# Performance work log

Hardware: AMD Instinct MI355X
Metric: run time of the kernel (lower is better)

The kernel has to match this reference:

```python
import jax, jax.numpy as jnp
import numpy as np

D_MODEL = 1024
NUM_HEADS = 16
DK = D_MODEL // NUM_HEADS  # 64


def setup_inputs() -> dict:
    key = jax.random.key(0)
    kx, kq, kk, kv, ko = jax.random.split(key, 5)
    B, S = 4, 2048
    # xavier-uniform-ish scale for square [d_model, d_model] matrices
    bound = float(np.sqrt(6.0 / (D_MODEL + D_MODEL)))
    uni = lambda k: jax.random.uniform(k, (D_MODEL, D_MODEL), jnp.float32, -bound, bound)
    return {
        "x": jax.random.normal(kx, (B, S, D_MODEL), jnp.float32),
        "q_heads": uni(kq),
        "k_heads": uni(kk),
        "v_heads": uni(kv),
        "output_proj": uni(ko),
    }


def reference(x, q_heads, k_heads, v_heads, output_proj):
    B, S, _ = x.shape
    # projections: x @ W.T, split into heads -> [B, H, S, dk]
    def proj(W):
        return (x @ W.T).reshape(B, S, NUM_HEADS, DK).transpose(0, 2, 1, 3)
    q, k, v = proj(q_heads), proj(k_heads), proj(v_heads)
    scale = 1.0 / jnp.sqrt(jnp.asarray(DK, x.dtype))
    scores = jnp.einsum("bhqd,bhkd->bhqk", q, k) * scale  # [B,H,S,S]
    causal = jnp.triu(jnp.ones((S, S), bool), k=1)
    scores = jnp.where(causal, jnp.asarray(-jnp.inf, scores.dtype), scores)
    attn = jax.nn.softmax(scores, axis=-1)
    out = jnp.einsum("bhqk,bhkd->bhqd", attn, v)  # [B,H,S,dk]
    out = out.transpose(0, 2, 1, 3).reshape(B, S, D_MODEL)
    return out @ output_proj.T
```

## Files before the change

kernel.cpp:

```cpp
#include <hip/hip_runtime.h>
#include <hip/hip_bf16.h>

#define AS1 __attribute__((address_space(1)))
#define AS3 __attribute__((address_space(3)))

typedef __hip_bfloat16 bf16;
typedef short bf16x8 __attribute__((ext_vector_type(8)));
typedef float f32x4 __attribute__((ext_vector_type(4)));

static constexpr int D = 1024, S = 2048, NB = 4, NH = 16, DK = 64;
static constexpr int M = NB * S;

__device__ __forceinline__ void gload16(void* lds_dst, const void* gsrc) {
  __builtin_amdgcn_global_load_lds((const AS1 void*)gsrc, (AS3 void*)lds_dst, 16, 0, 0);
}

__global__ void cvt_bf16_kernel(const float* __restrict__ src, bf16* __restrict__ dst, int n) {
  int i = (blockIdx.x * blockDim.x + threadIdx.x) * 4;
  int stride = gridDim.x * blockDim.x * 4;
  for (; i < n; i += stride) {
    float4 v = *(const float4*)(src + i);
    union { bf16 h[4]; uint2 u; } t;
    t.h[0] = __float2bfloat16(v.x);
    t.h[1] = __float2bfloat16(v.y);
    t.h[2] = __float2bfloat16(v.z);
    t.h[3] = __float2bfloat16(v.w);
    *(uint2*)(dst + i) = t.u;
  }
}

template <int MODE>
__global__ __launch_bounds__(256)
void gemm_bt(const bf16* __restrict__ A, const bf16* __restrict__ Bw,
             void* __restrict__ out, int K, int ldc, float scale) {
  __shared__ __align__(16) char lds[32768];
  char* Asm = lds;
  char* Bsm = lds + 16384;
  const int tid = threadIdx.x;
  const int w = tid >> 6, l = tid & 63;
  const int ql = l & 15, g = l >> 4;
  const int rowA = blockIdx.x * 128;
  const int rowB = blockIdx.y * 128;
  const int wr = (w >> 1) * 64, wc = (w & 1) * 64;

  f32x4 acc[4][4] = {};

  for (int k0 = 0; k0 < K; k0 += 64) {
#pragma unroll
    for (int i = 0; i < 4; ++i) {
      int o = ((i * 4 + w) << 10) + (l << 4);
      int row = o >> 7;
      int u = ((o >> 4) & 7) ^ (row & 7);
      gload16(Asm + ((i * 4 + w) << 10), A + (size_t)(rowA + row) * K + k0 + (u << 3));
      gload16(Bsm + ((i * 4 + w) << 10), Bw + (size_t)(rowB + row) * K + k0 + (u << 3));
    }
    __syncthreads();
#pragma unroll
    for (int kk = 0; kk < 2; ++kk) {
      bf16x8 af[4], bfr[4];
#pragma unroll
      for (int m = 0; m < 4; ++m) {
        int row = wr + m * 16 + ql;
        int sub = ((kk << 2) + g) ^ (row & 7);
        af[m] = *(const bf16x8*)(Asm + row * 128 + sub * 16);
      }
#pragma unroll
      for (int n = 0; n < 4; ++n) {
        int row = wc + n * 16 + ql;
        int sub = ((kk << 2) + g) ^ (row & 7);
        bfr[n] = *(const bf16x8*)(Bsm + row * 128 + sub * 16);
      }
#pragma unroll
      for (int m = 0; m < 4; ++m)
#pragma unroll
        for (int n = 0; n < 4; ++n)
          acc[m][n] = __builtin_amdgcn_mfma_f32_16x16x32_bf16(af[m], bfr[n], acc[m][n], 0, 0, 0);
    }
    __syncthreads();
  }

#pragma unroll
  for (int m = 0; m < 4; ++m)
#pragma unroll
    for (int n = 0; n < 4; ++n)
#pragma unroll
      for (int r = 0; r < 4; ++r) {
        int gm = rowA + wr + m * 16 + g * 4 + r;
        int gn = rowB + wc + n * 16 + ql;
        float v = acc[m][n][r] * scale;
        if (MODE == 0) {
          int b = gm >> 11, s = gm & 2047, h = gn >> 6, d = gn & 63;
          ((bf16*)out)[(((size_t)(b * 16 + h) * S) + s) * DK + d] = __float2bfloat16(v);
        } else if (MODE == 1) {
          int b = gn >> 11, s = gn & 2047;
          ((bf16*)out)[((size_t)b * 1024 + gm) * S + s] = __float2bfloat16(v);
        } else {
          ((float*)out)[(size_t)gm * ldc + gn] = v;
        }
      }
}

__global__ __launch_bounds__(256)
void attn_kernel(const bf16* __restrict__ Q, const bf16* __restrict__ Km,
                 const bf16* __restrict__ Vt, bf16* __restrict__ O) {
  __shared__ __align__(16) char P[4][2][2048];
  const int tid = threadIdx.x;
  const int w = tid >> 6, l = tid & 63;
  const int ql = l & 15, g = l >> 4;
  const int id = blockIdx.x;
  const int bh = (id & 7) + 8 * (id >> 6);
  const int x = (id >> 3) & 7;
  const int p = x + 8 * w;
  const int swz = (ql & 7) << 4;
  const float THR = 8.0f;

  const bf16* Qb = Q + (size_t)bh * S * DK;
  const bf16* Kb = Km + (size_t)bh * S * DK;
  const bf16* Vb = Vt + (size_t)bh * DK * S;
  const int bo = bh >> 4, hh = bh & 15;
  bf16* Ob = O + (size_t)bo * S * D + hh * 64;

  for (int round = 0; round < 2; ++round) {
    const int j = round ? 63 - p : p;
    const int qbase = j << 5;
    const int kv_end = qbase + 32;

    bf16x8 qf[2][2];
#pragma unroll
    for (int sub = 0; sub < 2; ++sub)
#pragma unroll
      for (int kk = 0; kk < 2; ++kk)
        qf[sub][kk] = *(const bf16x8*)(Qb + (size_t)(qbase + sub * 16 + ql) * DK + kk * 32 + g * 8);

    f32x4 oacc[2][4] = {};
    float mrow[2] = {-3e38f, -3e38f};
    float lrow[2] = {0.f, 0.f};

    bf16x8 kf[2][4];
#pragma unroll
    for (int kk = 0; kk < 2; ++kk)
#pragma unroll
      for (int mt = 0; mt < 4; ++mt)
        kf[kk][mt] = *(const bf16x8*)(Kb + (size_t)(mt * 16 + ql) * DK + kk * 32 + g * 8);

    for (int kv0 = 0; kv0 < kv_end; kv0 += 64) {
      const bool last = (kv0 + 64 >= kv_end);

      bf16x8 vf[2][4];
#pragma unroll
      for (int kk = 0; kk < 2; ++kk)
#pragma unroll
        for (int n = 0; n < 4; ++n)
          vf[kk][n] = *(const bf16x8*)(Vb + (size_t)(n * 16 + ql) * S + kv0 + kk * 32 + g * 8);

      f32x4 st[2][4];
#pragma unroll
      for (int sub = 0; sub < 2; ++sub)
#pragma unroll
        for (int mt = 0; mt < 4; ++mt) st[sub][mt] = f32x4{0.f, 0.f, 0.f, 0.f};
      __builtin_amdgcn_s_setprio(1);
#pragma unroll
      for (int kk = 0; kk < 2; ++kk)
#pragma unroll
        for (int sub = 0; sub < 2; ++sub)
#pragma unroll
          for (int mt = 0; mt < 4; ++mt)
            st[sub][mt] = __builtin_amdgcn_mfma_f32_16x16x32_bf16(kf[kk][mt], qf[sub][kk], st[sub][mt], 0, 0, 0);
      __builtin_amdgcn_s_setprio(0);

      if (!last) {
#pragma unroll
        for (int kk = 0; kk < 2; ++kk)
#pragma unroll
          for (int mt = 0; mt < 4; ++mt)
            kf[kk][mt] = *(const bf16x8*)(Kb + (size_t)(kv0 + 64 + mt * 16 + ql) * DK + kk * 32 + g * 8);
      }

#pragma unroll
      for (int sub = 0; sub < 2; ++sub) {
        const int qpos = qbase + sub * 16 + ql;
        if (last) {
#pragma unroll
          for (int mt = 0; mt < 4; ++mt)
#pragma unroll
            for (int r = 0; r < 4; ++r) {
              int kvpos = kv0 + mt * 16 + g * 4 + r;
              if (kvpos > qpos) st[sub][mt][r] = -3e38f;
            }
        }
        float tm[4];
#pragma unroll
        for (int mt = 0; mt < 4; ++mt)
          tm[mt] = fmaxf(fmaxf(st[sub][mt][0], st[sub][mt][1]),
                         fmaxf(st[sub][mt][2], st[sub][mt][3]));
        float tmax = fmaxf(fmaxf(tm[0], tm[1]), fmaxf(tm[2], tm[3]));
        if (__any(tmax > mrow[sub] + THR)) {
          float rm = tmax;
          rm = fmaxf(rm, __shfl_xor(rm, 16, 64));
          rm = fmaxf(rm, __shfl_xor(rm, 32, 64));
          float mnew = fmaxf(mrow[sub], rm);
          float sc = exp2f(mrow[sub] - mnew);
          mrow[sub] = mnew;
          lrow[sub] *= sc;
#pragma unroll
          for (int r = 0; r < 4; ++r) {
            float scr = __shfl(sc, g * 4 + r, 16);
#pragma unroll
            for (int n = 0; n < 4; ++n) oacc[sub][n][r] *= scr;
          }
        }
        float ps[4];
#pragma unroll
        for (int mt = 0; mt < 4; ++mt) {
          float e0 = exp2f(st[sub][mt][0] - mrow[sub]);
          float e1 = exp2f(st[sub][mt][1] - mrow[sub]);
          float e2 = exp2f(st[sub][mt][2] - mrow[sub]);
          float e3 = exp2f(st[sub][mt][3] - mrow[sub]);
          ps[mt] = (e0 + e1) + (e2 + e3);
          union { ushort us[4]; uint2 u; } pk;
          union { bf16 b; ushort u; } cv;
          cv.b = __float2bfloat16(e0); pk.us[0] = cv.u;
          cv.b = __float2bfloat16(e1); pk.us[1] = cv.u;
          cv.b = __float2bfloat16(e2); pk.us[2] = cv.u;
          cv.b = __float2bfloat16(e3); pk.us[3] = cv.u;
          *(uint2*)&P[w][sub][((ql << 7) + (mt << 5) + (g << 3)) ^ swz] = pk.u;
        }
        lrow[sub] += (ps[0] + ps[1]) + (ps[2] + ps[3]);
      }

      __builtin_amdgcn_s_setprio(1);
#pragma unroll
      for (int kk = 0; kk < 2; ++kk)
#pragma unroll
        for (int sub = 0; sub < 2; ++sub) {
          bf16x8 pa = *(const bf16x8*)&P[w][sub][((ql << 7) + (kk << 6) + (g << 4)) ^ swz];
#pragma unroll
          for (int n = 0; n < 4; ++n)
            oacc[sub][n] = __builtin_amdgcn_mfma_f32_16x16x32_bf16(pa, vf[kk][n], oacc[sub][n], 0, 0, 0);
        }
      __builtin_amdgcn_s_setprio(0);
    }

#pragma unroll
    for (int sub = 0; sub < 2; ++sub) {
      float lr = lrow[sub];
      lr += __shfl_xor(lr, 16, 64);
      lr += __shfl_xor(lr, 32, 64);
      float ldv[4];
#pragma unroll
      for (int r = 0; r < 4; ++r) ldv[r] = __shfl(lr, g * 4 + r, 16);
#pragma unroll
      for (int r = 0; r < 4; ++r) {
        int qrow = qbase + sub * 16 + g * 4 + r;
        float inv = 1.f / ldv[r];
#pragma unroll
        for (int n = 0; n < 4; ++n)
          Ob[(size_t)qrow * D + n * 16 + ql] = __float2bfloat16(oacc[sub][n][r] * inv);
      }
    }
  }
}

extern "C" void kernel_launch(void* const* d_in, const int* in_sizes, int n_in,
                              void* d_out, int out_size, void* d_ws, size_t ws_size,
                              hipStream_t stream) {
  const float* x  = (const float*)d_in[0];
  const float* wq = (const float*)d_in[1];
  const float* wk = (const float*)d_in[2];
  const float* wv = (const float*)d_in[3];
  const float* wo = (const float*)d_in[4];

  char* ws = (char*)d_ws;
  bf16* xb  = (bf16*)(ws);
  bf16* wqb = (bf16*)(ws + (16u << 20));
  bf16* wkb = (bf16*)(ws + (18u << 20));
  bf16* wvb = (bf16*)(ws + (20u << 20));
  bf16* wob = (bf16*)(ws + (22u << 20));
  bf16* Qb  = (bf16*)(ws + (24u << 20));
  bf16* Kb  = (bf16*)(ws + (40u << 20));
  bf16* Vtb = (bf16*)(ws + (56u << 20));
  bf16* Ob  = (bf16*)(ws + (72u << 20));

  cvt_bf16_kernel<<<2048, 256, 0, stream>>>(x, xb, M * D);
  cvt_bf16_kernel<<<1024, 256, 0, stream>>>(wq, wqb, D * D);
  cvt_bf16_kernel<<<1024, 256, 0, stream>>>(wk, wkb, D * D);
  cvt_bf16_kernel<<<1024, 256, 0, stream>>>(wv, wvb, D * D);
  cvt_bf16_kernel<<<1024, 256, 0, stream>>>(wo, wob, D * D);

  gemm_bt<0><<<dim3(M / 128, D / 128), 256, 0, stream>>>(xb, wqb, Qb, D, D, 0.18033688f);
  gemm_bt<0><<<dim3(M / 128, D / 128), 256, 0, stream>>>(xb, wkb, Kb, D, D, 1.0f);
  gemm_bt<1><<<dim3(D / 128, M / 128), 256, 0, stream>>>(wvb, xb, Vtb, D, D, 1.0f);

  attn_kernel<<<dim3(512), 256, 0, stream>>>(Qb, Kb, Vtb, Ob);

  gemm_bt<2><<<dim3(M / 128, D / 128), 256, 0, stream>>>(Ob, wob, d_out, D, D, 1.0f);
}
```

Measured before the change: 239.4 us.

## Split attention KV loop into two interleaved independent softmax streams per wave

Each wave now processes two independent online-softmax streams over the two halves of its KV range, calling a tile routine for each stream in turn and merging both partial results (max, sum, output) at the end. This gives the scheduler two independent dependency chains so MFMA, exp and memory latency from one stream can overlap with the other. The cost is doubled accumulator registers and doubled LDS for P. The explicit K-fragment prefetch into registers is dropped, and loads now happen inside each tile.

```diff
diff --git a/kernel.cpp b/kernel.cpp
--- a/kernel.cpp
+++ b/kernel.cpp
@@ -100,10 +100,112 @@
       }
 }
 
+struct SM2 {
+  f32x4 oacc[2][4];
+  float mrow[2];
+  float lrow[2];
+};
+
+__device__ __forceinline__ void attn_tile(
+    const bf16* __restrict__ Kb, const bf16* __restrict__ Vb, char* Pst,
+    const bf16x8 (&qf)[2][2], SM2& s, int kv0, int qbase, bool last,
+    int ql, int g, int swz) {
+  f32x4 st[2][4];
+#pragma unroll
+  for (int sub = 0; sub < 2; ++sub)
+#pragma unroll
+    for (int mt = 0; mt < 4; ++mt) st[sub][mt] = f32x4{0.f, 0.f, 0.f, 0.f};
+  __builtin_amdgcn_s_setprio(1);
+#pragma unroll
+  for (int kk = 0; kk < 2; ++kk) {
+    bf16x8 kf[4];
+#pragma unroll
+    for (int mt = 0; mt < 4; ++mt)
+      kf[mt] = *(const bf16x8*)(Kb + (size_t)(kv0 + mt * 16 + ql) * DK + kk * 32 + g * 8);
+#pragma unroll
+    for (int sub = 0; sub < 2; ++sub)
+#pragma unroll
+      for (int mt = 0; mt < 4; ++mt)
+        st[sub][mt] = __builtin_amdgcn_mfma_f32_16x16x32_bf16(kf[mt], qf[sub][kk], st[sub][mt], 0, 0, 0);
+  }
+  __builtin_amdgcn_s_setprio(0);
+
+#pragma unroll
+  for (int sub = 0; sub < 2; ++sub) {
+    const int qpos = qbase + sub * 16 + ql;
+    if (last) {
+#pragma unroll
+      for (int mt = 0; mt < 4; ++mt)
+#pragma unroll
+        for (int r = 0; r < 4; ++r) {
+          int kvpos = kv0 + mt * 16 + g * 4 + r;
+          if (kvpos > qpos) st[sub][mt][r] = -3e38f;
+        }
+    }
+    float tm[4];
+#pragma unroll
+    for (int mt = 0; mt < 4; ++mt)
+      tm[mt] = fmaxf(fmaxf(st[sub][mt][0], st[sub][mt][1]),
+                     fmaxf(st[sub][mt][2], st[sub][mt][3]));
+    float tmax = fmaxf(fmaxf(tm[0], tm[1]), fmaxf(tm[2], tm[3]));
+    if (__any(tmax > s.mrow[sub] + 8.0f)) {
+      float rm = tmax;
+      rm = fmaxf(rm, __shfl_xor(rm, 16, 64));
+      rm = fmaxf(rm, __shfl_xor(rm, 32, 64));
+      float mnew = fmaxf(s.mrow[sub], rm);
+      float sc = exp2f(s.mrow[sub] - mnew);
+      s.mrow[sub] = mnew;
+      s.lrow[sub] *= sc;
+#pragma unroll
+      for (int r = 0; r < 4; ++r) {
+        float scr = __shfl(sc, g * 4 + r, 16);
+#pragma unroll
+        for (int n = 0; n < 4; ++n) s.oacc[sub][n][r] *= scr;
+      }
+    }
+    float ps[4];
+#pragma unroll
+    for (int mt = 0; mt < 4; ++mt) {
+      float e0 = exp2f(st[sub][mt][0] - s.mrow[sub]);
+      float e1 = exp2f(st[sub][mt][1] - s.mrow[sub]);
+      float e2 = exp2f(st[sub][mt][2] - s.mrow[sub]);
+      float e3 = exp2f(st[sub][mt][3] - s.mrow[sub]);
+      ps[mt] = (e0 + e1) + (e2 + e3);
+      union { ushort us[4]; uint2 u; } pk;
+      union { bf16 b; ushort u; } cv;
+      cv.b = __float2bfloat16(e0); pk.us[0] = cv.u;
+      cv.b = __float2bfloat16(e1); pk.us[1] = cv.u;
+      cv.b = __float2bfloat16(e2); pk.us[2] = cv.u;
+      cv.b = __float2bfloat16(e3); pk.us[3] = cv.u;
+      *(uint2*)&Pst[(size_t)sub * 2048 + (((ql << 7) + (mt << 5) + (g << 3)) ^ swz)] = pk.u;
+    }
+    s.lrow[sub] += (ps[0] + ps[1]) + (ps[2] + ps[3]);
+  }
+
+  bf16x8 vf[2][4];
+#pragma unroll
+  for (int kk = 0; kk < 2; ++kk)
+#pragma unroll
+    for (int n = 0; n < 4; ++n)
+      vf[kk][n] = *(const bf16x8*)(Vb + (size_t)(n * 16 + ql) * S + kv0 + kk * 32 + g * 8);
+
+  __builtin_amdgcn_s_setprio(1);
+#pragma unroll
+  for (int kk = 0; kk < 2; ++kk)
+#pragma unroll
+    for (int sub = 0; sub < 2; ++sub) {
+      bf16x8 pa = *(const bf16x8*)&Pst[(size_t)sub * 2048 + (((ql << 7) + (kk << 6) + (g << 4)) ^ swz)];
+#pragma unroll
+      for (int n = 0; n < 4; ++n)
+        s.oacc[sub][n] = __builtin_amdgcn_mfma_f32_16x16x32_bf16(pa, vf[kk][n], s.oacc[sub][n], 0, 0, 0);
+    }
+  __builtin_amdgcn_s_setprio(0);
+}
+
 __global__ __launch_bounds__(256)
 void attn_kernel(const bf16* __restrict__ Q, const bf16* __restrict__ Km,
                  const bf16* __restrict__ Vt, bf16* __restrict__ O) {
-  __shared__ __align__(16) char P[4][2][2048];
+  __shared__ __align__(16) char P[4][2][2][2048];
   const int tid = threadIdx.x;
   const int w = tid >> 6, l = tid & 63;
   const int ql = l & 15, g = l >> 4;
@@ -112,7 +214,6 @@
   const int x = (id >> 3) & 7;
   const int p = x + 8 * w;
   const int swz = (ql & 7) << 4;
-  const float THR = 8.0f;
 
   const bf16* Qb = Q + (size_t)bh * S * DK;
   const bf16* Kb = Km + (size_t)bh * S * DK;
@@ -124,6 +225,8 @@
     const int j = round ? 63 - p : p;
     const int qbase = j << 5;
     const int kv_end = qbase + 32;
+    const int T = (kv_end + 63) >> 6;
+    const int nP = T >> 1;
 
     bf16x8 qf[2][2];
 #pragma unroll
@@ -132,130 +235,43 @@
       for (int kk = 0; kk < 2; ++kk)
         qf[sub][kk] = *(const bf16x8*)(Qb + (size_t)(qbase + sub * 16 + ql) * DK + kk * 32 + g * 8);
 
-    f32x4 oacc[2][4] = {};
-    float mrow[2] = {-3e38f, -3e38f};
-    float lrow[2] = {0.f, 0.f};
-
-    bf16x8 kf[2][4];
-#pragma unroll
-    for (int kk = 0; kk < 2; ++kk)
-#pragma unroll
-      for (int mt = 0; mt < 4; ++mt)
-        kf[kk][mt] = *(const bf16x8*)(Kb + (size_t)(mt * 16 + ql) * DK + kk * 32 + g * 8);
-
-    for (int kv0 = 0; kv0 < kv_end; kv0 += 64) {
-      const bool last = (kv0 + 64 >= kv_end);
-
-      bf16x8 vf[2][4];
-#pragma unroll
-      for (int kk = 0; kk < 2; ++kk)
-#pragma unroll
-        for (int n = 0; n < 4; ++n)
-          vf[kk][n] = *(const bf16x8*)(Vb + (size_t)(n * 16 + ql) * S + kv0 + kk * 32 + g * 8);
-
-      f32x4 st[2][4];
-#pragma unroll
-      for (int sub = 0; sub < 2; ++sub)
-#pragma unroll
-        for (int mt = 0; mt < 4; ++mt) st[sub][mt] = f32x4{0.f, 0.f, 0.f, 0.f};
-      __builtin_amdgcn_s_setprio(1);
-#pragma unroll
-      for (int kk = 0; kk < 2; ++kk)
-#pragma unroll
-        for (int sub = 0; sub < 2; ++sub)
-#pragma unroll
-          for (int mt = 0; mt < 4; ++mt)
-            st[sub][mt] = __builtin_amdgcn_mfma_f32_16x16x32_bf16(kf[kk][mt], qf[sub][kk], st[sub][mt], 0, 0, 0);
-      __builtin_amdgcn_s_setprio(0);
-
-      if (!last) {
-#pragma unroll
-        for (int kk = 0; kk < 2; ++kk)
-#pragma unroll
-          for (int mt = 0; mt < 4; ++mt)
-            kf[kk][mt] = *(const bf16x8*)(Kb + (size_t)(kv0 + 64 + mt * 16 + ql) * DK + kk * 32 + g * 8);
-      }
-
-#pragma unroll
-      for (int sub = 0; sub < 2; ++sub) {
-        const int qpos = qbase + sub * 16 + ql;
-        if (last) {
-#pragma unroll
-          for (int mt = 0; mt < 4; ++mt)
-#pragma unroll
-            for (int r = 0; r < 4; ++r) {
-              int kvpos = kv0 + mt * 16 + g * 4 + r;
-              if (kvpos > qpos) st[sub][mt][r] = -3e38f;
-            }
-        }
-        float tm[4];
-#pragma unroll
-        for (int mt = 0; mt < 4; ++mt)
-          tm[mt] = fmaxf(fmaxf(st[sub][mt][0], st[sub][mt][1]),
-                         fmaxf(st[sub][mt][2], st[sub][mt][3]));
-        float tmax = fmaxf(fmaxf(tm[0], tm[1]), fmaxf(tm[2], tm[3]));
-        if (__any(tmax > mrow[sub] + THR)) {
-          float rm = tmax;
-          rm = fmaxf(rm, __shfl_xor(rm, 16, 64));
-          rm = fmaxf(rm, __shfl_xor(rm, 32, 64));
-          float mnew = fmaxf(mrow[sub], rm);
-          float sc = exp2f(mrow[sub] - mnew);
-          mrow[sub] = mnew;
-          lrow[sub] *= sc;
-#pragma unroll
-          for (int r = 0; r < 4; ++r) {
-            float scr = __shfl(sc, g * 4 + r, 16);
-#pragma unroll
-            for (int n = 0; n < 4; ++n) oacc[sub][n][r] *= scr;
-          }
-        }
-        float ps[4];
-#pragma unroll
-        for (int mt = 0; mt < 4; ++mt) {
-          float e0 = exp2f(st[sub][mt][0] - mrow[sub]);
-          float e1 = exp2f(st[sub][mt][1] - mrow[sub]);
-          float e2 = exp2f(st[sub][mt][2] - mrow[sub]);
-          float e3 = exp2f(st[sub][mt][3] - mrow[sub]);
-          ps[mt] = (e0 + e1) + (e2 + e3);
-          union { ushort us[4]; uint2 u; } pk;
-          union { bf16 b; ushort u; } cv;
-          cv.b = __float2bfloat16(e0); pk.us[0] = cv.u;
-          cv.b = __float2bfloat16(e1); pk.us[1] = cv.u;
-          cv.b = __float2bfloat16(e2); pk.us[2] = cv.u;
-          cv.b = __float2bfloat16(e3); pk.us[3] = cv.u;
-          *(uint2*)&P[w][sub][((ql << 7) + (mt << 5) + (g << 3)) ^ swz] = pk.u;
-        }
-        lrow[sub] += (ps[0] + ps[1]) + (ps[2] + ps[3]);
-      }
-
-      __builtin_amdgcn_s_setprio(1);
-#pragma unroll
-      for (int kk = 0; kk < 2; ++kk)
-#pragma unroll
-        for (int sub = 0; sub < 2; ++sub) {
-          bf16x8 pa = *(const bf16x8*)&P[w][sub][((ql << 7) + (kk << 6) + (g << 4)) ^ swz];
-#pragma unroll
-          for (int n = 0; n < 4; ++n)
-            oacc[sub][n] = __builtin_amdgcn_mfma_f32_16x16x32_bf16(pa, vf[kk][n], oacc[sub][n], 0, 0, 0);
-        }
-      __builtin_amdgcn_s_setprio(0);
-    }
+    SM2 sA = {}, sB = {};
+    sA.mrow[0] = sA.mrow[1] = -3e38f;
+    sB.mrow[0] = sB.mrow[1] = -3e38f;
+    char* PA = &P[w][0][0][0];
+    char* PB = &P[w][1][0][0];
+
+    for (int i = 0; i < nP; ++i) {
+      attn_tile(Kb, Vb, PA, qf, sA, i << 6, qbase, false, ql, g, swz);
+      attn_tile(Kb, Vb, PB, qf, sB, (nP + i) << 6, qbase, (nP + i) == T - 1, ql, g, swz);
+    }
+    if (T & 1)
+      attn_tile(Kb, Vb, PA, qf, sA, (T - 1) << 6, qbase, true, ql, g, swz);
 
 #pragma unroll
     for (int sub = 0; sub < 2; ++sub) {
-      float lr = lrow[sub];
+      float m = fmaxf(sA.mrow[sub], sB.mrow[sub]);
+      float fA = exp2f(sA.mrow[sub] - m);
+      float fB = exp2f(sB.mrow[sub] - m);
+      float lr = fA * sA.lrow[sub] + fB * sB.lrow[sub];
       lr += __shfl_xor(lr, 16, 64);
       lr += __shfl_xor(lr, 32, 64);
-      float ldv[4];
-#pragma unroll
-      for (int r = 0; r < 4; ++r) ldv[r] = __shfl(lr, g * 4 + r, 16);
+      float ldv[4], fAr[4], fBr[4];
+#pragma unroll
+      for (int r = 0; r < 4; ++r) {
+        ldv[r] = __shfl(lr, g * 4 + r, 16);
+        fAr[r] = __shfl(fA, g * 4 + r, 16);
+        fBr[r] = __shfl(fB, g * 4 + r, 16);
+      }
 #pragma unroll
       for (int r = 0; r < 4; ++r) {
         int qrow = qbase + sub * 16 + g * 4 + r;
         float inv = 1.f / ldv[r];
 #pragma unroll
-        for (int n = 0; n < 4; ++n)
-          Ob[(size_t)qrow * D + n * 16 + ql] = __float2bfloat16(oacc[sub][n][r] * inv);
+        for (int n = 0; n < 4; ++n) {
+          float ov = fAr[r] * sA.oacc[sub][n][r] + fBr[r] * sB.oacc[sub][n][r];
+          Ob[(size_t)qrow * D + n * 16 + ql] = __float2bfloat16(ov * inv);
+        }
       }
     }
   }
```

Result: slower. 265.7 us (+11.0%).
